# Performance work log

Measured on AMD Instinct MI355X. Metric: run time of the kernel, lower is better.

## Reference

```python
import jax, jax.numpy as jnp
import numpy as np


def setup_inputs() -> dict:
    key = jax.random.key(0)
    kq, kk, kv = jax.random.split(key, 3)
    B, S, D = 32, 2048, 64  # (batch*heads, seq_len, head_dim)
    q = jax.random.normal(kq, (B, S, D), dtype=jnp.float32)
    k = jax.random.normal(kk, (B, S, D), dtype=jnp.float32)
    v = jax.random.normal(kv, (B, S, D), dtype=jnp.float32)
    return {"q": q, "k": k, "v": v}


def reference(q, k, v):
    # attention = q @ k^T  (no scale, no mask: defaults scale=None, attn_mask=None)
    scores = jnp.einsum("bqd,bkd->bqk", q, k)  # [B, S, S] materialized, as in source
    attn = jax.nn.softmax(scores, axis=2)      # Softmax(dim=2) == key axis for 3D
    # dropout is identity in eval / deterministic reference
    return jnp.einsum("bqk,bkd->bqd", attn, v)
```

## Files before the change

### kernel.cpp

```cpp
#include <hip/hip_runtime.h>
#include <stdint.h>

typedef __attribute__((ext_vector_type(4)))  float    f32x4;
typedef __attribute__((ext_vector_type(16))) float    f32x16;
typedef __attribute__((ext_vector_type(8)))  _Float16 f16x8;
typedef __attribute__((ext_vector_type(8)))  __bf16   bf16x8;

#define SEQ   2048
#define DH    64
#define BQ    128
#define BK    64
#define NT    (SEQ / BK)
#define HNT   (NT / 2)
#define ROWE  72
#define TILEE (64 * ROWE)
#define L2E   1.44269504088896340736f

#if __has_builtin(__builtin_amdgcn_exp2f)
static __device__ __forceinline__ float fast_exp2(float x) { return __builtin_amdgcn_exp2f(x); }
#else
static __device__ __forceinline__ float fast_exp2(float x) {
  float r; asm("v_exp_f32 %0, %1" : "=v"(r) : "v"(x)); return r;
}
#endif
static __device__ __forceinline__ uint32_t pack2_bf16(float a, float b) {
  union { __bf16 h[2]; uint32_t u; } cv;
  cv.h[0] = (__bf16)a; cv.h[1] = (__bf16)b;
  return cv.u;
}
union frag_u { uint32_t u[4]; bf16x8 v; };

typedef const __attribute__((address_space(1))) uint32_t* gp1_t;
typedef __attribute__((address_space(3))) uint32_t*       lp3_t;

__host__ __device__ inline int sigma32(int m) {
  int b = m & 3, h = (m >> 2) & 1, c = m >> 3;
  return ((c & 1) << 4) | (h << 3) | ((c >> 1) << 2) | b;
}

__global__ __launch_bounds__(256)
void prepass(const float* __restrict__ K, const float* __restrict__ V,
             _Float16* __restrict__ Kh, __bf16* __restrict__ Vh) {
  const int blk = blockIdx.x;
  const int tid = threadIdx.x;
  if (blk < 32 * NT) {
    const float* src = K + ((size_t)(blk >> 5) * SEQ + (size_t)(blk & 31) * 64) * DH;
    _Float16*    dst = Kh + (size_t)blk * TILEE;
    const int row = tid >> 2, c = (tid & 3) << 4;
    const int srow = (row & 32) | sigma32(row & 31);
    const float* sp = src + srow * DH + c;
    f32x4 x0 = *(const f32x4*)(sp + 0),  x1 = *(const f32x4*)(sp + 4);
    f32x4 x2 = *(const f32x4*)(sp + 8),  x3 = *(const f32x4*)(sp + 12);
    f16x8 h0, h1;
#pragma unroll
    for (int j = 0; j < 4; ++j) {
      h0[j] = (_Float16)x0[j]; h0[j + 4] = (_Float16)x1[j];
      h1[j] = (_Float16)x2[j]; h1[j + 4] = (_Float16)x3[j];
    }
    *(f16x8*)(dst + row * ROWE + c)     = h0;
    *(f16x8*)(dst + row * ROWE + c + 8) = h1;
  } else {
    const int blk2 = blk - 32 * NT;
    const float* src = V + ((size_t)(blk2 >> 5) * SEQ + (size_t)(blk2 & 31) * 64) * DH;
    __bf16*      dst = Vh + (size_t)blk2 * TILEE;
#pragma unroll
    for (int it = 0; it < 4; ++it) {
      int task = tid + it * 256;
      int d = task & 63, g = task >> 6;
      const float* sp = src + (size_t)(4 * g) * DH + d;
      __bf16 hv[4];
#pragma unroll
      for (int j = 0; j < 4; ++j) hv[j] = (__bf16)sp[(size_t)j * DH];
      *(uint64_t*)(dst + d * ROWE + 4 * g) = *(uint64_t*)hv;
    }
  }
}

__global__ __launch_bounds__(512, 2)
void flash_attn_v16(const float* __restrict__ Q, const _Float16* __restrict__ Kh,
                    const __bf16* __restrict__ Vh, float* __restrict__ O) {
  __shared__ _Float16 Ksb[2][2][64][ROWE];
  __shared__ __bf16   Vtb[2][2][64][ROWE];
  __shared__ float    Ls[4][32];

  const int tid  = threadIdx.x;
  const int wv   = tid >> 6;
  const int qw   = wv & 3;
  const int kh   = wv >> 2;
  const int lane = tid & 63;
  const int hfw  = lane >> 5;
  const int l31  = lane & 31;

  const int batch = blockIdx.x & 31;
  const int qblk  = blockIdx.x >> 5;

  const float* Qb = Q + (size_t)batch * SEQ * DH;
  float*       Ob = O + (size_t)batch * SEQ * DH;
  const uint32_t* Kt0 = (const uint32_t*)(Kh + (size_t)batch * NT * TILEE);
  const uint32_t* Vt0 = (const uint32_t*)(Vh + (size_t)batch * NT * TILEE);

  auto stage = [&](int t, int buf) {
    const uint32_t* kgp = Kt0 + (size_t)t * (TILEE / 2);
    const uint32_t* vgp = Vt0 + (size_t)t * (TILEE / 2);
    lp3_t kl = (lp3_t)&Ksb[kh][buf][0][0];
    lp3_t vl = (lp3_t)&Vtb[kh][buf][0][0];
#pragma unroll
    for (int j = qw; j < 9; j += 4) {
      __builtin_amdgcn_global_load_lds((gp1_t)(kgp + j * 256 + lane * 4), kl + j * 256, 16, 0, 0);
      __builtin_amdgcn_global_load_lds((gp1_t)(vgp + j * 256 + lane * 4), vl + j * 256, 16, 0, 0);
    }
  };

  const int qrow = qblk * BQ + qw * 32 + l31;
  f16x8 qf[4];
  {
    const float* qp = Qb + (size_t)qrow * DH + hfw * 8;
#pragma unroll
    for (int ks = 0; ks < 4; ++ks) {
      f32x4 a = *(const f32x4*)(qp + ks * 16);
      f32x4 b = *(const f32x4*)(qp + ks * 16 + 4);
#pragma unroll
      for (int j = 0; j < 4; ++j) {
        qf[ks][j]     = (_Float16)(a[j] * L2E);
        qf[ks][j + 4] = (_Float16)(b[j] * L2E);
      }
    }
  }

  f32x16 acc0 = {}, acc1 = {};
  float lsum = 0.f;

  const int t0 = kh * HNT;
  stage(t0, 0);

#pragma unroll 1
  for (int li = 0; li < HNT; ++li) {
    __syncthreads();
    if (li + 1 < HNT) stage(t0 + li + 1, (li + 1) & 1);
    const int buf = li & 1;

    __builtin_amdgcn_s_setprio(1);
    f32x16 s0 = {}, s1 = {};
#pragma unroll
    for (int ks = 0; ks < 4; ++ks) {
      int dof = ks * 16 + hfw * 8;
      f16x8 kf0 = *(const f16x8*)&Ksb[kh][buf][l31][dof];
      f16x8 kf1 = *(const f16x8*)&Ksb[kh][buf][l31 + 32][dof];
      s0 = __builtin_amdgcn_mfma_f32_32x32x16_f16(kf0, qf[ks], s0, 0, 0, 0);
      s1 = __builtin_amdgcn_mfma_f32_32x32x16_f16(kf1, qf[ks], s1, 0, 0, 0);
    }
    __builtin_amdgcn_s_setprio(0);

    frag_u fr[4];
#pragma unroll
    for (int t2 = 0; t2 < 2; ++t2) {
      const f32x16& s = t2 ? s1 : s0;
      float p[16];
#pragma unroll
      for (int j = 0; j < 16; ++j) p[j] = fast_exp2(s[j]);
      float a0 = (p[0] + p[1]) + (p[2] + p[3]);
      float a1 = (p[4] + p[5]) + (p[6] + p[7]);
      float a2 = (p[8] + p[9]) + (p[10] + p[11]);
      float a3 = (p[12] + p[13]) + (p[14] + p[15]);
      lsum += (a0 + a1) + (a2 + a3);
      fr[2 * t2    ].u[0] = pack2_bf16(p[0],  p[1]);
      fr[2 * t2    ].u[1] = pack2_bf16(p[2],  p[3]);
      fr[2 * t2    ].u[2] = pack2_bf16(p[8],  p[9]);
      fr[2 * t2    ].u[3] = pack2_bf16(p[10], p[11]);
      fr[2 * t2 + 1].u[0] = pack2_bf16(p[4],  p[5]);
      fr[2 * t2 + 1].u[1] = pack2_bf16(p[6],  p[7]);
      fr[2 * t2 + 1].u[2] = pack2_bf16(p[12], p[13]);
      fr[2 * t2 + 1].u[3] = pack2_bf16(p[14], p[15]);
    }

    __builtin_amdgcn_s_setprio(1);
#pragma unroll
    for (int ks = 0; ks < 4; ++ks) {
      int kof = ks * 16 + hfw * 8;
      bf16x8 v0 = *(const bf16x8*)&Vtb[kh][buf][l31][kof];
      bf16x8 v1 = *(const bf16x8*)&Vtb[kh][buf][l31 + 32][kof];
      acc0 = __builtin_amdgcn_mfma_f32_32x32x16_bf16(fr[ks].v, v0, acc0, 0, 0, 0);
      acc1 = __builtin_amdgcn_mfma_f32_32x32x16_bf16(fr[ks].v, v1, acc1, 0, 0, 0);
    }
    __builtin_amdgcn_s_setprio(0);
  }

  float tot = lsum + __shfl_xor(lsum, 32);
  __syncthreads();
  float* cb = (float*)&Ksb[0][0][0][0];
  float* sb = (float*)&Vtb[0][0][0][0];
  if (kh == 1) {
    const int base = (qw * 64 + lane) * 33;
#pragma unroll
    for (int j = 0; j < 16; ++j) {
      cb[base + j]      = acc0[j];
      cb[base + j + 16] = acc1[j];
    }
    sb[qw * 64 + lane] = tot;
  }
  __syncthreads();
  if (kh == 0) {
    const int base = (qw * 64 + lane) * 33;
    float tot2 = tot + sb[qw * 64 + lane];
    Ls[qw][l31] = __builtin_amdgcn_rcpf(tot2);
#pragma unroll
    for (int j = 0; j < 16; ++j) {
      acc0[j] += cb[base + j];
      acc1[j] += cb[base + j + 16];
    }
#pragma unroll
    for (int j = 0; j < 16; ++j) {
      int row = (j & 3) + 8 * (j >> 2) + 4 * hfw;
      float inv = Ls[qw][row];
      size_t off = (size_t)(qblk * BQ + qw * 32 + row) * DH + l31;
      Ob[off]      = acc0[j] * inv;
      Ob[off + 32] = acc1[j] * inv;
    }
  }
}

extern "C" void kernel_launch(void* const* d_in, const int* in_sizes, int n_in,
                              void* d_out, int out_size, void* d_ws, size_t ws_size,
                              hipStream_t stream) {
  (void)in_sizes; (void)n_in; (void)ws_size; (void)out_size;
  const float* q = (const float*)d_in[0];
  const float* k = (const float*)d_in[1];
  const float* v = (const float*)d_in[2];
  float* o = (float*)d_out;
  _Float16* Kh = (_Float16*)d_ws;
  __bf16*   Vh = (__bf16*)((char*)d_ws + (size_t)32 * NT * TILEE * sizeof(_Float16));

  prepass<<<dim3(2 * 32 * NT), dim3(256), 0, stream>>>(k, v, Kh, Vh);
  flash_attn_v16<<<dim3(32 * (SEQ / BQ)), dim3(512), 0, stream>>>(q, Kh, Vh, o);
}
```

Before: 139.5 us.

## Fuse K/V conversion prepass into attention kernel with global flag sync

Removes the separate prepass launch. Each attention block now converts two K/V tiles of its batch to fp16/bf16 in the workspace, publishes per-tile flags, and spin-waits with a bounded loop on the flags of all tiles in its batch. Any tiles still missing after the loop are converted redundantly by the waiting block. This is meant to save a kernel launch and its gap, at the cost of a hipMemsetAsync, atomic polling, and possible redundant conversion work when blocks are not co-resident.

```diff
diff --git a/kernel.cpp b/kernel.cpp
--- a/kernel.cpp
+++ b/kernel.cpp
@@ -38,50 +38,45 @@
   return ((c & 1) << 4) | (h << 3) | ((c >> 1) << 2) | b;
 }
 
-__global__ __launch_bounds__(256)
-void prepass(const float* __restrict__ K, const float* __restrict__ V,
-             _Float16* __restrict__ Kh, __bf16* __restrict__ Vh) {
-  const int blk = blockIdx.x;
-  const int tid = threadIdx.x;
-  if (blk < 32 * NT) {
-    const float* src = K + ((size_t)(blk >> 5) * SEQ + (size_t)(blk & 31) * 64) * DH;
-    _Float16*    dst = Kh + (size_t)blk * TILEE;
-    const int row = tid >> 2, c = (tid & 3) << 4;
-    const int srow = (row & 32) | sigma32(row & 31);
-    const float* sp = src + srow * DH + c;
-    f32x4 x0 = *(const f32x4*)(sp + 0),  x1 = *(const f32x4*)(sp + 4);
-    f32x4 x2 = *(const f32x4*)(sp + 8),  x3 = *(const f32x4*)(sp + 12);
-    f16x8 h0, h1;
-#pragma unroll
-    for (int j = 0; j < 4; ++j) {
-      h0[j] = (_Float16)x0[j]; h0[j + 4] = (_Float16)x1[j];
-      h1[j] = (_Float16)x2[j]; h1[j + 4] = (_Float16)x3[j];
-    }
-    *(f16x8*)(dst + row * ROWE + c)     = h0;
-    *(f16x8*)(dst + row * ROWE + c + 8) = h1;
-  } else {
-    const int blk2 = blk - 32 * NT;
-    const float* src = V + ((size_t)(blk2 >> 5) * SEQ + (size_t)(blk2 & 31) * 64) * DH;
-    __bf16*      dst = Vh + (size_t)blk2 * TILEE;
-#pragma unroll
-    for (int it = 0; it < 4; ++it) {
-      int task = tid + it * 256;
-      int d = task & 63, g = task >> 6;
-      const float* sp = src + (size_t)(4 * g) * DH + d;
-      __bf16 hv[4];
-#pragma unroll
-      for (int j = 0; j < 4; ++j) hv[j] = (__bf16)sp[(size_t)j * DH];
-      *(uint64_t*)(dst + d * ROWE + 4 * g) = *(uint64_t*)hv;
-    }
+static __device__ __forceinline__ void convK_tile(const float* __restrict__ src,
+                                                  _Float16* __restrict__ dst, int t) {
+  const int row = t >> 2, c = (t & 3) << 4;
+  const int srow = (row & 32) | sigma32(row & 31);
+  const float* sp = src + srow * DH + c;
+  f32x4 x0 = *(const f32x4*)(sp + 0),  x1 = *(const f32x4*)(sp + 4);
+  f32x4 x2 = *(const f32x4*)(sp + 8),  x3 = *(const f32x4*)(sp + 12);
+  f16x8 h0, h1;
+#pragma unroll
+  for (int j = 0; j < 4; ++j) {
+    h0[j] = (_Float16)x0[j]; h0[j + 4] = (_Float16)x1[j];
+    h1[j] = (_Float16)x2[j]; h1[j + 4] = (_Float16)x3[j];
+  }
+  *(f16x8*)(dst + row * ROWE + c)     = h0;
+  *(f16x8*)(dst + row * ROWE + c + 8) = h1;
+}
+static __device__ __forceinline__ void convV_tile(const float* __restrict__ src,
+                                                  __bf16* __restrict__ dst, int t) {
+#pragma unroll
+  for (int it = 0; it < 4; ++it) {
+    int task = t + it * 256;
+    int d = task & 63, g = task >> 6;
+    const float* sp = src + (size_t)(4 * g) * DH + d;
+    __bf16 hv[4];
+#pragma unroll
+    for (int j = 0; j < 4; ++j) hv[j] = (__bf16)sp[(size_t)j * DH];
+    *(uint64_t*)(dst + d * ROWE + 4 * g) = *(uint64_t*)hv;
   }
 }
 
 __global__ __launch_bounds__(512, 2)
-void flash_attn_v16(const float* __restrict__ Q, const _Float16* __restrict__ Kh,
-                    const __bf16* __restrict__ Vh, float* __restrict__ O) {
+void flash_attn_v17(const float* __restrict__ Q, const float* __restrict__ K,
+                    const float* __restrict__ V, _Float16* __restrict__ Kh,
+                    __bf16* __restrict__ Vh, unsigned* __restrict__ flags,
+                    float* __restrict__ O) {
   __shared__ _Float16 Ksb[2][2][64][ROWE];
   __shared__ __bf16   Vtb[2][2][64][ROWE];
   __shared__ float    Ls[4][32];
+  __shared__ unsigned missMask;
 
   const int tid  = threadIdx.x;
   const int wv   = tid >> 6;
@@ -94,10 +89,64 @@
   const int batch = blockIdx.x & 31;
   const int qblk  = blockIdx.x >> 5;
 
-  const float* Qb = Q + (size_t)batch * SEQ * DH;
-  float*       Ob = O + (size_t)batch * SEQ * DH;
-  const uint32_t* Kt0 = (const uint32_t*)(Kh + (size_t)batch * NT * TILEE);
-  const uint32_t* Vt0 = (const uint32_t*)(Vh + (size_t)batch * NT * TILEE);
+  const float* Qb  = Q + (size_t)batch * SEQ * DH;
+  const float* Kr  = K + (size_t)batch * SEQ * DH;
+  const float* Vr  = V + (size_t)batch * SEQ * DH;
+  float*       Ob  = O + (size_t)batch * SEQ * DH;
+  _Float16*    KhB = Kh + (size_t)batch * NT * TILEE;
+  __bf16*      VhB = Vh + (size_t)batch * NT * TILEE;
+  unsigned*    fb  = flags + batch * NT;
+
+  {
+    const int myt = 2 * qblk + (tid >> 8);
+    const int t8  = tid & 255;
+    convK_tile(Kr + (size_t)myt * 64 * DH, KhB + (size_t)myt * TILEE, t8);
+    convV_tile(Vr + (size_t)myt * 64 * DH, VhB + (size_t)myt * TILEE, t8);
+  }
+  __threadfence();
+  __syncthreads();
+  if (tid < 2) atomicExch(&fb[2 * qblk + tid], 1u);
+
+  const int qrow = qblk * BQ + qw * 32 + l31;
+  f16x8 qf[4];
+  {
+    const float* qp = Qb + (size_t)qrow * DH + hfw * 8;
+#pragma unroll
+    for (int ks = 0; ks < 4; ++ks) {
+      f32x4 a = *(const f32x4*)(qp + ks * 16);
+      f32x4 b = *(const f32x4*)(qp + ks * 16 + 4);
+#pragma unroll
+      for (int j = 0; j < 4; ++j) {
+        qf[ks][j]     = (_Float16)(a[j] * L2E);
+        qf[ks][j + 4] = (_Float16)(b[j] * L2E);
+      }
+    }
+  }
+
+  if (tid == 0) missMask = 0u;
+  __syncthreads();
+  if (tid < NT) {
+    bool ok = false;
+    for (int sp = 0; sp < 1000 && !ok; ++sp)
+      ok = (atomicAdd(&fb[tid], 0u) != 0u);
+    if (!ok) atomicOr(&missMask, 1u << tid);
+  }
+  __syncthreads();
+  {
+    unsigned mm = missMask;
+    if (mm) {
+      while (mm) {
+        int t = __ffs(mm) - 1; mm &= mm - 1;
+        convK_tile(Kr + (size_t)t * 64 * DH, KhB + (size_t)t * TILEE, tid & 255);
+        convV_tile(Vr + (size_t)t * 64 * DH, VhB + (size_t)t * TILEE, tid & 255);
+      }
+      __threadfence();
+    }
+  }
+  __syncthreads();
+
+  const uint32_t* Kt0 = (const uint32_t*)KhB;
+  const uint32_t* Vt0 = (const uint32_t*)VhB;
 
   auto stage = [&](int t, int buf) {
     const uint32_t* kgp = Kt0 + (size_t)t * (TILEE / 2);
@@ -110,22 +159,6 @@
       __builtin_amdgcn_global_load_lds((gp1_t)(vgp + j * 256 + lane * 4), vl + j * 256, 16, 0, 0);
     }
   };
-
-  const int qrow = qblk * BQ + qw * 32 + l31;
-  f16x8 qf[4];
-  {
-    const float* qp = Qb + (size_t)qrow * DH + hfw * 8;
-#pragma unroll
-    for (int ks = 0; ks < 4; ++ks) {
-      f32x4 a = *(const f32x4*)(qp + ks * 16);
-      f32x4 b = *(const f32x4*)(qp + ks * 16 + 4);
-#pragma unroll
-      for (int j = 0; j < 4; ++j) {
-        qf[ks][j]     = (_Float16)(a[j] * L2E);
-        qf[ks][j + 4] = (_Float16)(b[j] * L2E);
-      }
-    }
-  }
 
   f32x16 acc0 = {}, acc1 = {};
   float lsum = 0.f;
@@ -227,9 +260,11 @@
   const float* k = (const float*)d_in[1];
   const float* v = (const float*)d_in[2];
   float* o = (float*)d_out;
-  _Float16* Kh = (_Float16*)d_ws;
-  __bf16*   Vh = (__bf16*)((char*)d_ws + (size_t)32 * NT * TILEE * sizeof(_Float16));
-
-  prepass<<<dim3(2 * 32 * NT), dim3(256), 0, stream>>>(k, v, Kh, Vh);
-  flash_attn_v16<<<dim3(32 * (SEQ / BQ)), dim3(512), 0, stream>>>(q, Kh, Vh, o);
-}
+  const size_t kvbytes = (size_t)32 * NT * TILEE * sizeof(_Float16);
+  _Float16* Kh    = (_Float16*)d_ws;
+  __bf16*   Vh    = (__bf16*)((char*)d_ws + kvbytes);
+  unsigned* flags = (unsigned*)((char*)d_ws + 2 * kvbytes);
+
+  hipMemsetAsync(flags, 0, (size_t)32 * NT * sizeof(unsigned), stream);
+  flash_attn_v17<<<dim3(32 * (SEQ / BQ)), dim3(512), 0, stream>>>(q, k, v, Kh, Vh, flags, o);
+}
```

After: 297.8 us. +113.4%, slower.

## Fuse K/V fp32-to-half conversion into attention kernel, drop prepass

Applied to the files above, without the earlier changes.

Removes the separate prepass kernel that converted K to fp16 and V to transposed bf16 in workspace. Each attention block now loads fp32 K/V tiles into registers during the current tile's compute, converts them, and writes the next LDS buffer after the PV MFMAs. This saves a kernel launch and the workspace round trip. In exchange, each of the 16 query blocks per batch re-reads and re-converts the full fp32 K/V, doubling global bytes per tile, and register pressure rises. The V loads are scalar strided reads.

```diff
diff --git a/kernel.cpp b/kernel.cpp
--- a/kernel.cpp
+++ b/kernel.cpp
@@ -13,7 +13,6 @@
 #define NT    (SEQ / BK)
 #define HNT   (NT / 2)
 #define ROWE  72
-#define TILEE (64 * ROWE)
 #define L2E   1.44269504088896340736f
 
 #if __has_builtin(__builtin_amdgcn_exp2f)
@@ -30,55 +29,14 @@
 }
 union frag_u { uint32_t u[4]; bf16x8 v; };
 
-typedef const __attribute__((address_space(1))) uint32_t* gp1_t;
-typedef __attribute__((address_space(3))) uint32_t*       lp3_t;
-
 __host__ __device__ inline int sigma32(int m) {
   int b = m & 3, h = (m >> 2) & 1, c = m >> 3;
   return ((c & 1) << 4) | (h << 3) | ((c >> 1) << 2) | b;
 }
 
-__global__ __launch_bounds__(256)
-void prepass(const float* __restrict__ K, const float* __restrict__ V,
-             _Float16* __restrict__ Kh, __bf16* __restrict__ Vh) {
-  const int blk = blockIdx.x;
-  const int tid = threadIdx.x;
-  if (blk < 32 * NT) {
-    const float* src = K + ((size_t)(blk >> 5) * SEQ + (size_t)(blk & 31) * 64) * DH;
-    _Float16*    dst = Kh + (size_t)blk * TILEE;
-    const int row = tid >> 2, c = (tid & 3) << 4;
-    const int srow = (row & 32) | sigma32(row & 31);
-    const float* sp = src + srow * DH + c;
-    f32x4 x0 = *(const f32x4*)(sp + 0),  x1 = *(const f32x4*)(sp + 4);
-    f32x4 x2 = *(const f32x4*)(sp + 8),  x3 = *(const f32x4*)(sp + 12);
-    f16x8 h0, h1;
-#pragma unroll
-    for (int j = 0; j < 4; ++j) {
-      h0[j] = (_Float16)x0[j]; h0[j + 4] = (_Float16)x1[j];
-      h1[j] = (_Float16)x2[j]; h1[j + 4] = (_Float16)x3[j];
-    }
-    *(f16x8*)(dst + row * ROWE + c)     = h0;
-    *(f16x8*)(dst + row * ROWE + c + 8) = h1;
-  } else {
-    const int blk2 = blk - 32 * NT;
-    const float* src = V + ((size_t)(blk2 >> 5) * SEQ + (size_t)(blk2 & 31) * 64) * DH;
-    __bf16*      dst = Vh + (size_t)blk2 * TILEE;
-#pragma unroll
-    for (int it = 0; it < 4; ++it) {
-      int task = tid + it * 256;
-      int d = task & 63, g = task >> 6;
-      const float* sp = src + (size_t)(4 * g) * DH + d;
-      __bf16 hv[4];
-#pragma unroll
-      for (int j = 0; j < 4; ++j) hv[j] = (__bf16)sp[(size_t)j * DH];
-      *(uint64_t*)(dst + d * ROWE + 4 * g) = *(uint64_t*)hv;
-    }
-  }
-}
-
 __global__ __launch_bounds__(512, 2)
-void flash_attn_v16(const float* __restrict__ Q, const _Float16* __restrict__ Kh,
-                    const __bf16* __restrict__ Vh, float* __restrict__ O) {
+void flash_attn_v18(const float* __restrict__ Q, const float* __restrict__ K,
+                    const float* __restrict__ V, float* __restrict__ O) {
   __shared__ _Float16 Ksb[2][2][64][ROWE];
   __shared__ __bf16   Vtb[2][2][64][ROWE];
   __shared__ float    Ls[4][32];
@@ -95,19 +53,43 @@
   const int qblk  = blockIdx.x >> 5;
 
   const float* Qb = Q + (size_t)batch * SEQ * DH;
+  const float* Kr = K + (size_t)batch * SEQ * DH;
+  const float* Vr = V + (size_t)batch * SEQ * DH;
   float*       Ob = O + (size_t)batch * SEQ * DH;
-  const uint32_t* Kt0 = (const uint32_t*)(Kh + (size_t)batch * NT * TILEE);
-  const uint32_t* Vt0 = (const uint32_t*)(Vh + (size_t)batch * NT * TILEE);
-
-  auto stage = [&](int t, int buf) {
-    const uint32_t* kgp = Kt0 + (size_t)t * (TILEE / 2);
-    const uint32_t* vgp = Vt0 + (size_t)t * (TILEE / 2);
-    lp3_t kl = (lp3_t)&Ksb[kh][buf][0][0];
-    lp3_t vl = (lp3_t)&Vtb[kh][buf][0][0];
-#pragma unroll
-    for (int j = qw; j < 9; j += 4) {
-      __builtin_amdgcn_global_load_lds((gp1_t)(kgp + j * 256 + lane * 4), kl + j * 256, 16, 0, 0);
-      __builtin_amdgcn_global_load_lds((gp1_t)(vgp + j * 256 + lane * 4), vl + j * 256, 16, 0, 0);
+
+  const int t8    = qw * 64 + lane;
+  const int krow  = t8 >> 2;
+  const int kc    = (t8 & 3) << 4;
+  const int ksrow = (krow & 32) | sigma32(krow & 31);
+  const float* kbase = Kr + (size_t)ksrow * DH + kc;
+
+  auto convLoad = [&](int t, f32x4* kx, float (*vx)[4]) {
+    const float* kp = kbase + (size_t)t * 64 * DH;
+#pragma unroll
+    for (int u = 0; u < 4; ++u) kx[u] = *(const f32x4*)(kp + 4 * u);
+    const float* vp0 = Vr + (size_t)t * 64 * DH + lane;
+#pragma unroll
+    for (int it = 0; it < 4; ++it) {
+      const float* vp = vp0 + (size_t)(4 * (qw + 4 * it)) * DH;
+#pragma unroll
+      for (int j = 0; j < 4; ++j) vx[it][j] = vp[(size_t)j * DH];
+    }
+  };
+  auto convWrite = [&](int buf, const f32x4* kx, const float (*vx)[4]) {
+    f16x8 h0, h1;
+#pragma unroll
+    for (int j = 0; j < 4; ++j) {
+      h0[j] = (_Float16)kx[0][j]; h0[j + 4] = (_Float16)kx[1][j];
+      h1[j] = (_Float16)kx[2][j]; h1[j + 4] = (_Float16)kx[3][j];
+    }
+    *(f16x8*)&Ksb[kh][buf][krow][kc]     = h0;
+    *(f16x8*)&Ksb[kh][buf][krow][kc + 8] = h1;
+#pragma unroll
+    for (int it = 0; it < 4; ++it) {
+      __bf16 hv[4];
+#pragma unroll
+      for (int j = 0; j < 4; ++j) hv[j] = (__bf16)vx[it][j];
+      *(uint64_t*)&Vtb[kh][buf][lane][4 * (qw + 4 * it)] = *(uint64_t*)hv;
     }
   };
 
@@ -131,13 +113,16 @@
   float lsum = 0.f;
 
   const int t0 = kh * HNT;
-  stage(t0, 0);
+
+  f32x4 kx[4]; float vx[4][4];
+  convLoad(t0, kx, vx);
+  convWrite(0, kx, vx);
 
 #pragma unroll 1
   for (int li = 0; li < HNT; ++li) {
     __syncthreads();
-    if (li + 1 < HNT) stage(t0 + li + 1, (li + 1) & 1);
     const int buf = li & 1;
+    if (li + 1 < HNT) convLoad(t0 + li + 1, kx, vx);
 
     __builtin_amdgcn_s_setprio(1);
     f32x16 s0 = {}, s1 = {};
@@ -183,6 +168,8 @@
       acc1 = __builtin_amdgcn_mfma_f32_32x32x16_bf16(fr[ks].v, v1, acc1, 0, 0, 0);
     }
     __builtin_amdgcn_s_setprio(0);
+
+    if (li + 1 < HNT) convWrite(buf ^ 1, kx, vx);
   }
 
   float tot = lsum + __shfl_xor(lsum, 32);
@@ -222,14 +209,10 @@
 extern "C" void kernel_launch(void* const* d_in, const int* in_sizes, int n_in,
                               void* d_out, int out_size, void* d_ws, size_t ws_size,
                               hipStream_t stream) {
-  (void)in_sizes; (void)n_in; (void)ws_size; (void)out_size;
+  (void)in_sizes; (void)n_in; (void)d_ws; (void)ws_size; (void)out_size;
   const float* q = (const float*)d_in[0];
   const float* k = (const float*)d_in[1];
   const float* v = (const float*)d_in[2];
   float* o = (float*)d_out;
-  _Float16* Kh = (_Float16*)d_ws;
-  __bf16*   Vh = (__bf16*)((char*)d_ws + (size_t)32 * NT * TILEE * sizeof(_Float16));
-
-  prepass<<<dim3(2 * 32 * NT), dim3(256), 0, stream>>>(k, v, Kh, Vh);
-  flash_attn_v16<<<dim3(32 * (SEQ / BQ)), dim3(512), 0, stream>>>(q, Kh, Vh, o);
-}
+  flash_attn_v18<<<dim3(32 * (SEQ / BQ)), dim3(512), 0, stream>>>(q, k, v, o);
+}
```

Measured after the change: 137.1 us. No clear change (-1.8%).
